# Kernel optimization log

Measured on AMD Instinct MI355X. Metric: run time of the kernel, lower is better.

The kernel has to match this reference:

```python
import jax, jax.numpy as jnp
import numpy as np

N = 100000  # nodes
NEG_SLOPE = 0.2


def gat_conv(x, W, att_src, att_dst, bias, src, dst):
    # x: [N, Fin], W: [Fin, Fout], att_*: [Fout], bias: [Fout]
    h = x @ W                                    # [N, Fout]
    a_s = h @ att_src                            # [N]
    a_d = h @ att_dst                            # [N]
    e = jax.nn.leaky_relu(a_s[src] + a_d[dst], NEG_SLOPE)  # [E]
    # segment softmax over destination-node neighborhoods
    m = jax.ops.segment_max(e, dst, num_segments=N)        # [N]
    ex = jnp.exp(e - m[dst])
    denom = jax.ops.segment_sum(ex, dst, num_segments=N)   # [N]
    alpha = ex / denom[dst]                      # [E]
    out = jax.ops.segment_sum(alpha[:, None] * h[src], dst, num_segments=N)
    return out + bias


def setup_inputs() -> dict:
    key = jax.random.key(0)
    ks = jax.random.split(key, 10)
    F_in, H, C, E = 512, 16, 40, 3200000
    x = jax.random.normal(ks[0], (N, F_in), dtype=jnp.float32)
    edge_index = jax.random.randint(ks[1], (2, E), 0, N, dtype=jnp.int64)
    s1 = 1.0 / np.sqrt(F_in)
    s2 = 1.0 / np.sqrt(H)
    return {
        "x": x,
        "W1": jax.random.normal(ks[2], (F_in, H), dtype=jnp.float32) * s1,
        "att_src1": jax.random.normal(ks[3], (H,), dtype=jnp.float32) * s2,
        "att_dst1": jax.random.normal(ks[4], (H,), dtype=jnp.float32) * s2,
        "bias1": jnp.zeros((H,), dtype=jnp.float32),
        "W2": jax.random.normal(ks[5], (H, C), dtype=jnp.float32) * s2,
        "att_src2": jax.random.normal(ks[6], (C,), dtype=jnp.float32) / np.sqrt(C),
        "att_dst2": jax.random.normal(ks[7], (C,), dtype=jnp.float32) / np.sqrt(C),
        "bias2": jnp.zeros((C,), dtype=jnp.float32),
        "edge_index": edge_index,
    }


def reference(x, W1, att_src1, att_dst1, bias1, W2, att_src2, att_dst2, bias2, edge_index):
    # add self loops (PyG GATConv default add_self_loops=True)
    loop = jnp.arange(N, dtype=edge_index.dtype)
    src = jnp.concatenate([edge_index[0], loop])
    dst = jnp.concatenate([edge_index[1], loop])
    h = gat_conv(x, W1, att_src1, att_dst1, bias1, src, dst)
    h = jax.nn.relu(h)  # dropout is identity in eval mode
    out = gat_conv(h, W2, att_src2, att_dst2, bias2, src, dst)
    return out
```

## Files before the change

kernel.cpp:

```cpp
#include <hip/hip_runtime.h>
#include <math.h>


constexpr int FIN = 512;
constexpr int F1  = 16;
constexpr int C2  = 40;
constexpr float SLOPE = 0.2f;
constexpr int BSH  = 8;
constexpr int NBMAX = 512;

__global__ __launch_bounds__(128) void k1_gemm(
    const float* __restrict__ x, const float* __restrict__ W1,
    const float* __restrict__ att_s, const float* __restrict__ att_d,
    float* __restrict__ h1, float* __restrict__ a_s, float* __restrict__ a_d, int n)
{
    __shared__ float WT[F1][FIN + 4];
    for (int idx = threadIdx.x; idx < FIN * F1; idx += 128) {
        int k = idx >> 4, o = idx & 15;
        WT[o][k] = W1[idx];
    }
    __syncthreads();

    const int o0 = (threadIdx.x & 3) * 4;
    const int ng = threadIdx.x >> 2;
    const int node0 = blockIdx.x * 128 + ng * 4;

    const float* xr[4];
#pragma unroll
    for (int nn = 0; nn < 4; ++nn) {
        int node = node0 + nn;
        xr[nn] = x + (size_t)(node < n ? node : 0) * FIN;
    }

    float acc[4][4] = {};
    for (int k = 0; k < FIN; k += 4) {
        float4 wv[4];
#pragma unroll
        for (int oo = 0; oo < 4; ++oo) wv[oo] = *(const float4*)&WT[o0 + oo][k];
#pragma unroll
        for (int nn = 0; nn < 4; ++nn) {
            float4 xv = *(const float4*)(xr[nn] + k);
#pragma unroll
            for (int oo = 0; oo < 4; ++oo)
                acc[nn][oo] += xv.x * wv[oo].x + xv.y * wv[oo].y +
                               xv.z * wv[oo].z + xv.w * wv[oo].w;
        }
    }

#pragma unroll
    for (int nn = 0; nn < 4; ++nn) {
        int node = node0 + nn;
        float ps = 0.f, pd = 0.f;
#pragma unroll
        for (int oo = 0; oo < 4; ++oo) {
            ps += acc[nn][oo] * att_s[o0 + oo];
            pd += acc[nn][oo] * att_d[o0 + oo];
        }
        ps += __shfl_xor(ps, 1); ps += __shfl_xor(ps, 2);
        pd += __shfl_xor(pd, 1); pd += __shfl_xor(pd, 2);
        if (node < n) {
            *(float4*)&h1[(size_t)node * F1 + o0] =
                make_float4(acc[nn][0], acc[nn][1], acc[nn][2], acc[nn][3]);
            if ((threadIdx.x & 3) == 0) { a_s[node] = ps; a_d[node] = pd; }
        }
    }
}

__global__ __launch_bounds__(256) void k_bhist(const int* __restrict__ dst,
                                               int* __restrict__ bcnt, int E, int nb)
{
    __shared__ int cnt[NBMAX];
    for (int t = threadIdx.x; t < NBMAX; t += 256) cnt[t] = 0;
    __syncthreads();
    int base = blockIdx.x * 4096;
#pragma unroll
    for (int k = 0; k < 16; ++k) {
        int e = base + k * 256 + threadIdx.x;
        if (e < E) atomicAdd(&cnt[dst[e] >> BSH], 1);
    }
    __syncthreads();
    for (int t = threadIdx.x; t < nb; t += 256) {
        int c = cnt[t];
        if (c) atomicAdd(&bcnt[t], c);
    }
}

__global__ __launch_bounds__(512) void k_bscan(const int* __restrict__ bcnt,
                                               int* __restrict__ bbase,
                                               int* __restrict__ gcur, int nb, int E)
{
    __shared__ int sc[512];
    int t = threadIdx.x;
    int v = (t < nb) ? bcnt[t] : 0;
    sc[t] = v; __syncthreads();
    for (int off = 1; off < 512; off <<= 1) {
        int u = (t >= off) ? sc[t - off] : 0;
        __syncthreads();
        sc[t] += u;
        __syncthreads();
    }
    int excl = sc[t] - v;
    if (t < nb) { bbase[t] = excl; gcur[t] = excl; }
    if (t == 0) bbase[nb] = E;
}

__global__ __launch_bounds__(256) void k_bucket(const int* __restrict__ src,
                                                const int* __restrict__ dst,
                                                int* __restrict__ gcur,
                                                unsigned int* __restrict__ bpk, int E)
{
    __shared__ int cnt[NBMAX];
    __shared__ int cur[NBMAX];
    for (int t = threadIdx.x; t < NBMAX; t += 256) cnt[t] = 0;
    __syncthreads();
    int base = blockIdx.x * 4096;
#pragma unroll
    for (int k = 0; k < 16; ++k) {
        int e = base + k * 256 + threadIdx.x;
        if (e < E) atomicAdd(&cnt[dst[e] >> BSH], 1);
    }
    __syncthreads();
    for (int t = threadIdx.x; t < NBMAX; t += 256) {
        int c = cnt[t];
        cur[t] = c ? atomicAdd(&gcur[t], c) : 0;
    }
    __syncthreads();
#pragma unroll
    for (int k = 0; k < 16; ++k) {
        int e = base + k * 256 + threadIdx.x;
        if (e < E) {
            int d = dst[e];
            int b = d >> BSH;
            int pos = atomicAdd(&cur[b], 1);
            bpk[pos] = (unsigned)src[e] | ((unsigned)(d & ((1 << BSH) - 1)) << 17);
        }
    }
}

__global__ __launch_bounds__(256) void k_refine(const unsigned int* __restrict__ bpk,
                                                const int* __restrict__ bbase,
                                                int* __restrict__ offs,
                                                int* __restrict__ ssrc, int n, int E)
{
    __shared__ int cnt[256];
    __shared__ int sc[256];
    int b = blockIdx.x;
    int beg = bbase[b], end = bbase[b + 1];
    int t = threadIdx.x;
    cnt[t] = 0;
    __syncthreads();
    for (int j = beg + t; j < end; j += 256)
        atomicAdd(&cnt[(bpk[j] >> 17) & 255], 1);
    __syncthreads();
    int v = cnt[t];
    sc[t] = v; __syncthreads();
    for (int off = 1; off < 256; off <<= 1) {
        int u = (t >= off) ? sc[t - off] : 0;
        __syncthreads();
        sc[t] += u;
        __syncthreads();
    }
    int excl = sc[t] - v;
    int node = (b << BSH) + t;
    if (node < n) offs[node] = beg + excl;
    __syncthreads();
    cnt[t] = excl;
    __syncthreads();
    for (int j = beg + t; j < end; j += 256) {
        unsigned pk = bpk[j];
        int local = (pk >> 17) & 255;
        int pos = atomicAdd(&cnt[local], 1);
        ssrc[beg + pos] = (int)(pk & 0x1FFFFu);
    }
    if (b == (int)gridDim.x - 1 && t == 0) offs[n] = E;
}

__global__ __launch_bounds__(256) void g1_gather(
    const int* __restrict__ offs, const int* __restrict__ ssrc,
    const float* __restrict__ h1, const float* __restrict__ a_s, const float* __restrict__ a_d,
    const float* __restrict__ bias1, const float* __restrict__ W2,
    const float* __restrict__ att_s2, const float* __restrict__ att_d2,
    float* __restrict__ hin2, float* __restrict__ pa_s, float* __restrict__ pa_d, int n)
{
    __shared__ float vs[F1], vd[F1];
    if (threadIdx.x < 32) {
        int f = threadIdx.x & 15;
        const float* att = (threadIdx.x < 16) ? att_s2 : att_d2;
        float sum = 0.f;
        for (int c = 0; c < C2; ++c) sum += W2[f * C2 + c] * att[c];
        if (threadIdx.x < 16) vs[f] = sum; else vd[f] = sum;
    }
    __syncthreads();
    const int g = threadIdx.x >> 4, f = threadIdx.x & 15;
    const int i = blockIdx.x * 16 + g;
    if (i >= n) return;
    const float adi = a_d[i];
    float acc = 0.f, dacc = 0.f;
    const int jb = offs[i], je = offs[i + 1];
    for (int j0 = jb; j0 < je; j0 += 16) {
        const int rem = je - j0;
        int se = ssrc[(f < rem) ? j0 + f : jb];
        float ev = a_s[se] + adi;
        ev = (ev >= 0.f) ? ev : SLOPE * ev;
        float pex = (f < rem) ? __expf(ev) : 0.f;
        dacc += pex;
        if (rem >= 16) {
#pragma unroll
            for (int t = 0; t < 16; ++t) {
                int s = __shfl(se, t, 16);
                float ex = __shfl(pex, t, 16);
                acc += ex * h1[(size_t)s * F1 + f];
            }
        } else {
            for (int t = 0; t < rem; ++t) {
                int s = __shfl(se, t, 16);
                float ex = __shfl(pex, t, 16);
                acc += ex * h1[(size_t)s * F1 + f];
            }
        }
    }
    float evs = a_s[i] + adi;
    evs = (evs >= 0.f) ? evs : SLOPE * evs;
    float exs = __expf(evs);
    acc += exs * h1[(size_t)i * F1 + f];
    float den = dacc;
#pragma unroll
    for (int o = 1; o < 16; o <<= 1) den += __shfl_xor(den, o);
    den += exs;
    float val = fmaxf(acc / den + bias1[f], 0.f);
    hin2[(size_t)i * F1 + f] = val;
    float ps = val * vs[f], pd = val * vd[f];
#pragma unroll
    for (int o = 1; o < 16; o <<= 1) { ps += __shfl_xor(ps, o); pd += __shfl_xor(pd, o); }
    if (f == 0) { pa_s[i] = ps; pa_d[i] = pd; }
}

__global__ __launch_bounds__(256) void g2_gather(
    const int* __restrict__ offs, const int* __restrict__ ssrc,
    const float* __restrict__ hin2, const float* __restrict__ a_s, const float* __restrict__ a_d,
    const float* __restrict__ W2, const float* __restrict__ bias2,
    float* __restrict__ out, int n)
{
    __shared__ float W2s[F1 * 41];
    __shared__ float vals[16][17];
    for (int idx = threadIdx.x; idx < F1 * C2; idx += 256)
        W2s[(idx / C2) * 41 + (idx % C2)] = W2[idx];
    __syncthreads();
    const int g = threadIdx.x >> 4, f = threadIdx.x & 15;
    const int i = blockIdx.x * 16 + g;
    if (i >= n) return;
    const float adi = a_d[i];
    float acc = 0.f, dacc = 0.f;
    const int jb = offs[i], je = offs[i + 1];
    for (int j0 = jb; j0 < je; j0 += 16) {
        const int rem = je - j0;
        int se = ssrc[(f < rem) ? j0 + f : jb];
        float ev = a_s[se] + adi;
        ev = (ev >= 0.f) ? ev : SLOPE * ev;
        float pex = (f < rem) ? __expf(ev) : 0.f;
        dacc += pex;
        if (rem >= 16) {
#pragma unroll
            for (int t = 0; t < 16; ++t) {
                int s = __shfl(se, t, 16);
                float ex = __shfl(pex, t, 16);
                acc += ex * hin2[(size_t)s * F1 + f];
            }
        } else {
            for (int t = 0; t < rem; ++t) {
                int s = __shfl(se, t, 16);
                float ex = __shfl(pex, t, 16);
                acc += ex * hin2[(size_t)s * F1 + f];
            }
        }
    }
    float evs = a_s[i] + adi;
    evs = (evs >= 0.f) ? evs : SLOPE * evs;
    float exs = __expf(evs);
    acc += exs * hin2[(size_t)i * F1 + f];
    float den = dacc;
#pragma unroll
    for (int o = 1; o < 16; o <<= 1) den += __shfl_xor(den, o);
    den += exs;
    vals[g][f] = acc / den;
    for (int c = f; c < C2; c += 16) {
        float r = bias2[c];
#pragma unroll
        for (int ff = 0; ff < F1; ++ff) r += vals[g][ff] * W2s[ff * 41 + c];
        out[(size_t)i * C2 + c] = r;
    }
}

extern "C" void kernel_launch(void* const* d_in, const int* in_sizes, int n_in,
                              void* d_out, int out_size, void* d_ws, size_t ws_size,
                              hipStream_t stream) {
    const float* x      = (const float*)d_in[0];
    const float* W1     = (const float*)d_in[1];
    const float* att_s1 = (const float*)d_in[2];
    const float* att_d1 = (const float*)d_in[3];
    const float* bias1  = (const float*)d_in[4];
    const float* W2     = (const float*)d_in[5];
    const float* att_s2 = (const float*)d_in[6];
    const float* att_d2 = (const float*)d_in[7];
    const float* bias2  = (const float*)d_in[8];
    const int*   edge   = (const int*)d_in[9];

    const int n = in_sizes[0] / FIN;
    const int E = in_sizes[9] / 2;
    const int* src = edge;
    const int* dst = edge + E;
    const int NBK = (n + (1 << BSH) - 1) >> BSH;

    size_t Ns = (size_t)n, Es = (size_t)E;
    int*   ssrc  = (int*)d_ws;
    int*   offs  = ssrc + Es;
    int*   bcnt  = offs + Ns + 1;
    int*   bbase = bcnt + NBMAX;
    int*   gcur  = bbase + NBMAX + 1;
    unsigned int* bpk = (unsigned int*)(gcur + NBMAX);
    float* h1    = (float*)bpk;
    float* a_s1  = h1   + 16 * Ns;
    float* a_d1  = a_s1 + Ns;
    float* hin2  = a_d1 + Ns;
    float* pa_s2 = hin2 + 16 * Ns;
    float* pa_d2 = pa_s2 + Ns;
    float* out   = (float*)d_out;

    const int gbA = (E + 4095) / 4096;
    const int gb1 = (n + 127) / 128;
    const int gbg = (n + 15) / 16;

    hipMemsetAsync(bcnt, 0, sizeof(int) * NBMAX, stream);
    k_bhist <<<gbA, 256, 0, stream>>>(dst, bcnt, E, NBK);
    k_bscan <<<1, 512, 0, stream>>>(bcnt, bbase, gcur, NBK, E);
    k_bucket<<<gbA, 256, 0, stream>>>(src, dst, gcur, bpk, E);
    k_refine<<<NBK, 256, 0, stream>>>(bpk, bbase, offs, ssrc, n, E);
    k1_gemm <<<gb1, 128, 0, stream>>>(x, W1, att_s1, att_d1, h1, a_s1, a_d1, n);
    g1_gather<<<gbg, 256, 0, stream>>>(offs, ssrc, h1, a_s1, a_d1, bias1, W2,
                                       att_s2, att_d2, hin2, pa_s2, pa_d2, n);
    g2_gather<<<gbg, 256, 0, stream>>>(offs, ssrc, hin2, pa_s2, pa_d2, W2, bias2, out, n);
}
```

Baseline: 613.8 us.

## Fuse per-bucket CSR refine into aggregation kernels using LDS-local edge lists

Removes the separate refine kernel that wrote a global CSR. Each aggregation kernel now rebuilds its bucket's per-node edge list in shared memory, with one thread per node accumulating all 16 features using float4 loads. It falls back to scanning the whole bucket when the edge count exceeds LDS capacity. This drops the global ssrc/offs writes and reads, but the bucket sort is redone twice. With only NBK (~391) blocks of 256 threads and about 40KB of LDS each, occupancy and load balance may suffer, and the per-thread serial loops follow skewed degrees.

```diff
diff --git a/kernel.cpp b/kernel.cpp
--- a/kernel.cpp
+++ b/kernel.cpp
@@ -6,8 +6,9 @@
 constexpr int F1  = 16;
 constexpr int C2  = 40;
 constexpr float SLOPE = 0.2f;
-constexpr int BSH  = 8;
+constexpr int BSH   = 8;
 constexpr int NBMAX = 512;
+constexpr int LDSE  = 9728;
 
 __global__ __launch_bounds__(128) void k1_gemm(
     const float* __restrict__ x, const float* __restrict__ W1,
@@ -137,157 +138,245 @@
     }
 }
 
-__global__ __launch_bounds__(256) void k_refine(const unsigned int* __restrict__ bpk,
-                                                const int* __restrict__ bbase,
-                                                int* __restrict__ offs,
-                                                int* __restrict__ ssrc, int n, int E)
-{
-    __shared__ int cnt[256];
-    __shared__ int sc[256];
-    int b = blockIdx.x;
-    int beg = bbase[b], end = bbase[b + 1];
-    int t = threadIdx.x;
-    cnt[t] = 0;
-    __syncthreads();
-    for (int j = beg + t; j < end; j += 256)
-        atomicAdd(&cnt[(bpk[j] >> 17) & 255], 1);
-    __syncthreads();
-    int v = cnt[t];
-    sc[t] = v; __syncthreads();
-    for (int off = 1; off < 256; off <<= 1) {
-        int u = (t >= off) ? sc[t - off] : 0;
-        __syncthreads();
-        sc[t] += u;
-        __syncthreads();
-    }
-    int excl = sc[t] - v;
-    int node = (b << BSH) + t;
-    if (node < n) offs[node] = beg + excl;
-    __syncthreads();
-    cnt[t] = excl;
-    __syncthreads();
-    for (int j = beg + t; j < end; j += 256) {
-        unsigned pk = bpk[j];
-        int local = (pk >> 17) & 255;
-        int pos = atomicAdd(&cnt[local], 1);
-        ssrc[beg + pos] = (int)(pk & 0x1FFFFu);
-    }
-    if (b == (int)gridDim.x - 1 && t == 0) offs[n] = E;
-}
-
-__global__ __launch_bounds__(256) void g1_gather(
-    const int* __restrict__ offs, const int* __restrict__ ssrc,
+__global__ __launch_bounds__(256) void f1_agg(
+    const unsigned int* __restrict__ bpk, const int* __restrict__ bbase,
     const float* __restrict__ h1, const float* __restrict__ a_s, const float* __restrict__ a_d,
     const float* __restrict__ bias1, const float* __restrict__ W2,
     const float* __restrict__ att_s2, const float* __restrict__ att_d2,
     float* __restrict__ hin2, float* __restrict__ pa_s, float* __restrict__ pa_d, int n)
 {
-    __shared__ float vs[F1], vd[F1];
-    if (threadIdx.x < 32) {
-        int f = threadIdx.x & 15;
-        const float* att = (threadIdx.x < 16) ? att_s2 : att_d2;
+    __shared__ int lsrc[LDSE];
+    __shared__ int cnt[256];
+    __shared__ int scn[256];
+    __shared__ float vs[F1], vd[F1], bl[F1];
+    const int b = blockIdx.x, t = threadIdx.x;
+    const int beg = bbase[b], end = bbase[b + 1];
+    const int m = end - beg;
+
+    if (t < 32) {
+        int f = t & 15;
+        const float* att = (t < 16) ? att_s2 : att_d2;
         float sum = 0.f;
         for (int c = 0; c < C2; ++c) sum += W2[f * C2 + c] * att[c];
-        if (threadIdx.x < 16) vs[f] = sum; else vd[f] = sum;
-    }
-    __syncthreads();
-    const int g = threadIdx.x >> 4, f = threadIdx.x & 15;
-    const int i = blockIdx.x * 16 + g;
-    if (i >= n) return;
-    const float adi = a_d[i];
-    float acc = 0.f, dacc = 0.f;
-    const int jb = offs[i], je = offs[i + 1];
-    for (int j0 = jb; j0 < je; j0 += 16) {
-        const int rem = je - j0;
-        int se = ssrc[(f < rem) ? j0 + f : jb];
-        float ev = a_s[se] + adi;
-        ev = (ev >= 0.f) ? ev : SLOPE * ev;
-        float pex = (f < rem) ? __expf(ev) : 0.f;
-        dacc += pex;
-        if (rem >= 16) {
-#pragma unroll
-            for (int t = 0; t < 16; ++t) {
-                int s = __shfl(se, t, 16);
-                float ex = __shfl(pex, t, 16);
-                acc += ex * h1[(size_t)s * F1 + f];
+        if (t < 16) vs[f] = sum; else vd[f] = sum;
+    } else if (t < 48) {
+        bl[t - 32] = bias1[t - 32];
+    }
+    cnt[t] = 0;
+    __syncthreads();
+
+    int myBeg = 0, myCnt = 0;
+    const bool fits = (m <= LDSE);
+    if (fits) {
+        for (int j = beg + t; j < end; j += 256)
+            atomicAdd(&cnt[(bpk[j] >> 17) & 255], 1);
+        __syncthreads();
+        int v = cnt[t];
+        scn[t] = v;
+        __syncthreads();
+        for (int off = 1; off < 256; off <<= 1) {
+            int u = (t >= off) ? scn[t - off] : 0;
+            __syncthreads();
+            scn[t] += u;
+            __syncthreads();
+        }
+        myCnt = v;
+        myBeg = scn[t] - v;
+        cnt[t] = myBeg;
+        __syncthreads();
+        for (int j = beg + t; j < end; j += 256) {
+            unsigned pk = bpk[j];
+            int p = atomicAdd(&cnt[(pk >> 17) & 255], 1);
+            lsrc[p] = (int)(pk & 0x1FFFFu);
+        }
+        __syncthreads();
+    }
+
+    const int node = (b << BSH) + t;
+    if (node >= n) return;
+
+    const float adi = a_d[node];
+    float acc[F1];
+#pragma unroll
+    for (int f = 0; f < F1; ++f) acc[f] = 0.f;
+    float den = 0.f;
+
+    if (fits) {
+        for (int k = 0; k < myCnt; ++k) {
+            int s = lsrc[myBeg + k];
+            float ev = a_s[s] + adi;
+            ev = (ev >= 0.f) ? ev : SLOPE * ev;
+            float ex = __expf(ev);
+            den += ex;
+            const float4* hp = (const float4*)(h1 + (size_t)s * F1);
+#pragma unroll
+            for (int q = 0; q < 4; ++q) {
+                float4 v = hp[q];
+                acc[4*q+0] += ex * v.x; acc[4*q+1] += ex * v.y;
+                acc[4*q+2] += ex * v.z; acc[4*q+3] += ex * v.w;
             }
-        } else {
-            for (int t = 0; t < rem; ++t) {
-                int s = __shfl(se, t, 16);
-                float ex = __shfl(pex, t, 16);
-                acc += ex * h1[(size_t)s * F1 + f];
+        }
+    } else {
+        for (int j = beg; j < end; ++j) {
+            unsigned pk = bpk[j];
+            if ((int)((pk >> 17) & 255) != t) continue;
+            int s = (int)(pk & 0x1FFFFu);
+            float ev = a_s[s] + adi;
+            ev = (ev >= 0.f) ? ev : SLOPE * ev;
+            float ex = __expf(ev);
+            den += ex;
+            const float4* hp = (const float4*)(h1 + (size_t)s * F1);
+#pragma unroll
+            for (int q = 0; q < 4; ++q) {
+                float4 v = hp[q];
+                acc[4*q+0] += ex * v.x; acc[4*q+1] += ex * v.y;
+                acc[4*q+2] += ex * v.z; acc[4*q+3] += ex * v.w;
             }
         }
     }
-    float evs = a_s[i] + adi;
+
+    float evs = a_s[node] + adi;
     evs = (evs >= 0.f) ? evs : SLOPE * evs;
     float exs = __expf(evs);
-    acc += exs * h1[(size_t)i * F1 + f];
-    float den = dacc;
-#pragma unroll
-    for (int o = 1; o < 16; o <<= 1) den += __shfl_xor(den, o);
-    den += exs;
-    float val = fmaxf(acc / den + bias1[f], 0.f);
-    hin2[(size_t)i * F1 + f] = val;
-    float ps = val * vs[f], pd = val * vd[f];
-#pragma unroll
-    for (int o = 1; o < 16; o <<= 1) { ps += __shfl_xor(ps, o); pd += __shfl_xor(pd, o); }
-    if (f == 0) { pa_s[i] = ps; pa_d[i] = pd; }
-}
-
-__global__ __launch_bounds__(256) void g2_gather(
-    const int* __restrict__ offs, const int* __restrict__ ssrc,
+    const float4* hs = (const float4*)(h1 + (size_t)node * F1);
+    float inv;
+    {
+        float d2 = den + exs;
+        inv = 1.f / d2;
+    }
+    float ps = 0.f, pd = 0.f;
+    float4* ho = (float4*)(hin2 + (size_t)node * F1);
+#pragma unroll
+    for (int q = 0; q < 4; ++q) {
+        float4 sv = hs[q];
+        float4 V;
+        V.x = fmaxf((acc[4*q+0] + exs * sv.x) * inv + bl[4*q+0], 0.f);
+        V.y = fmaxf((acc[4*q+1] + exs * sv.y) * inv + bl[4*q+1], 0.f);
+        V.z = fmaxf((acc[4*q+2] + exs * sv.z) * inv + bl[4*q+2], 0.f);
+        V.w = fmaxf((acc[4*q+3] + exs * sv.w) * inv + bl[4*q+3], 0.f);
+        ho[q] = V;
+        ps += V.x * vs[4*q+0] + V.y * vs[4*q+1] + V.z * vs[4*q+2] + V.w * vs[4*q+3];
+        pd += V.x * vd[4*q+0] + V.y * vd[4*q+1] + V.z * vd[4*q+2] + V.w * vd[4*q+3];
+    }
+    pa_s[node] = ps; pa_d[node] = pd;
+}
+
+__global__ __launch_bounds__(256) void f2_agg(
+    const unsigned int* __restrict__ bpk, const int* __restrict__ bbase,
     const float* __restrict__ hin2, const float* __restrict__ a_s, const float* __restrict__ a_d,
     const float* __restrict__ W2, const float* __restrict__ bias2,
     float* __restrict__ out, int n)
 {
-    __shared__ float W2s[F1 * 41];
-    __shared__ float vals[16][17];
-    for (int idx = threadIdx.x; idx < F1 * C2; idx += 256)
-        W2s[(idx / C2) * 41 + (idx % C2)] = W2[idx];
-    __syncthreads();
-    const int g = threadIdx.x >> 4, f = threadIdx.x & 15;
-    const int i = blockIdx.x * 16 + g;
-    if (i >= n) return;
-    const float adi = a_d[i];
-    float acc = 0.f, dacc = 0.f;
-    const int jb = offs[i], je = offs[i + 1];
-    for (int j0 = jb; j0 < je; j0 += 16) {
-        const int rem = je - j0;
-        int se = ssrc[(f < rem) ? j0 + f : jb];
-        float ev = a_s[se] + adi;
-        ev = (ev >= 0.f) ? ev : SLOPE * ev;
-        float pex = (f < rem) ? __expf(ev) : 0.f;
-        dacc += pex;
-        if (rem >= 16) {
-#pragma unroll
-            for (int t = 0; t < 16; ++t) {
-                int s = __shfl(se, t, 16);
-                float ex = __shfl(pex, t, 16);
-                acc += ex * hin2[(size_t)s * F1 + f];
+    __shared__ int lsrc[LDSE];
+    __shared__ int cnt[256];
+    __shared__ int scn[256];
+    __shared__ float W2s[F1 * C2];
+    __shared__ float b2[C2];
+    const int b = blockIdx.x, t = threadIdx.x;
+    const int beg = bbase[b], end = bbase[b + 1];
+    const int m = end - beg;
+
+    for (int idx = t; idx < F1 * C2; idx += 256) W2s[idx] = W2[idx];
+    if (t < C2) b2[t] = bias2[t];
+    cnt[t] = 0;
+    __syncthreads();
+
+    int myBeg = 0, myCnt = 0;
+    const bool fits = (m <= LDSE);
+    if (fits) {
+        for (int j = beg + t; j < end; j += 256)
+            atomicAdd(&cnt[(bpk[j] >> 17) & 255], 1);
+        __syncthreads();
+        int v = cnt[t];
+        scn[t] = v;
+        __syncthreads();
+        for (int off = 1; off < 256; off <<= 1) {
+            int u = (t >= off) ? scn[t - off] : 0;
+            __syncthreads();
+            scn[t] += u;
+            __syncthreads();
+        }
+        myCnt = v;
+        myBeg = scn[t] - v;
+        cnt[t] = myBeg;
+        __syncthreads();
+        for (int j = beg + t; j < end; j += 256) {
+            unsigned pk = bpk[j];
+            int p = atomicAdd(&cnt[(pk >> 17) & 255], 1);
+            lsrc[p] = (int)(pk & 0x1FFFFu);
+        }
+        __syncthreads();
+    }
+
+    const int node = (b << BSH) + t;
+    if (node >= n) return;
+
+    const float adi = a_d[node];
+    float acc[F1];
+#pragma unroll
+    for (int f = 0; f < F1; ++f) acc[f] = 0.f;
+    float den = 0.f;
+
+    if (fits) {
+        for (int k = 0; k < myCnt; ++k) {
+            int s = lsrc[myBeg + k];
+            float ev = a_s[s] + adi;
+            ev = (ev >= 0.f) ? ev : SLOPE * ev;
+            float ex = __expf(ev);
+            den += ex;
+            const float4* hp = (const float4*)(hin2 + (size_t)s * F1);
+#pragma unroll
+            for (int q = 0; q < 4; ++q) {
+                float4 v = hp[q];
+                acc[4*q+0] += ex * v.x; acc[4*q+1] += ex * v.y;
+                acc[4*q+2] += ex * v.z; acc[4*q+3] += ex * v.w;
             }
-        } else {
-            for (int t = 0; t < rem; ++t) {
-                int s = __shfl(se, t, 16);
-                float ex = __shfl(pex, t, 16);
-                acc += ex * hin2[(size_t)s * F1 + f];
+        }
+    } else {
+        for (int j = beg; j < end; ++j) {
+            unsigned pk = bpk[j];
+            if ((int)((pk >> 17) & 255) != t) continue;
+            int s = (int)(pk & 0x1FFFFu);
+            float ev = a_s[s] + adi;
+            ev = (ev >= 0.f) ? ev : SLOPE * ev;
+            float ex = __expf(ev);
+            den += ex;
+            const float4* hp = (const float4*)(hin2 + (size_t)s * F1);
+#pragma unroll
+            for (int q = 0; q < 4; ++q) {
+                float4 v = hp[q];
+                acc[4*q+0] += ex * v.x; acc[4*q+1] += ex * v.y;
+                acc[4*q+2] += ex * v.z; acc[4*q+3] += ex * v.w;
             }
         }
     }
-    float evs = a_s[i] + adi;
+
+    float evs = a_s[node] + adi;
     evs = (evs >= 0.f) ? evs : SLOPE * evs;
     float exs = __expf(evs);
-    acc += exs * hin2[(size_t)i * F1 + f];
-    float den = dacc;
-#pragma unroll
-    for (int o = 1; o < 16; o <<= 1) den += __shfl_xor(den, o);
-    den += exs;
-    vals[g][f] = acc / den;
-    for (int c = f; c < C2; c += 16) {
-        float r = bias2[c];
-#pragma unroll
-        for (int ff = 0; ff < F1; ++ff) r += vals[g][ff] * W2s[ff * 41 + c];
-        out[(size_t)i * C2 + c] = r;
+    const float4* hs = (const float4*)(hin2 + (size_t)node * F1);
+    float inv = 1.f / (den + exs);
+    float val[F1];
+#pragma unroll
+    for (int q = 0; q < 4; ++q) {
+        float4 sv = hs[q];
+        val[4*q+0] = (acc[4*q+0] + exs * sv.x) * inv;
+        val[4*q+1] = (acc[4*q+1] + exs * sv.y) * inv;
+        val[4*q+2] = (acc[4*q+2] + exs * sv.z) * inv;
+        val[4*q+3] = (acc[4*q+3] + exs * sv.w) * inv;
+    }
+    float* op = out + (size_t)node * C2;
+    for (int c0 = 0; c0 < C2; c0 += 4) {
+        float4 r = make_float4(b2[c0], b2[c0+1], b2[c0+2], b2[c0+3]);
+#pragma unroll
+        for (int f = 0; f < F1; ++f) {
+            float v = val[f];
+            r.x += v * W2s[f * C2 + c0 + 0];
+            r.y += v * W2s[f * C2 + c0 + 1];
+            r.z += v * W2s[f * C2 + c0 + 2];
+            r.w += v * W2s[f * C2 + c0 + 3];
+        }
+        *(float4*)(op + c0) = r;
     }
 }
 
@@ -311,32 +400,28 @@
     const int* dst = edge + E;
     const int NBK = (n + (1 << BSH) - 1) >> BSH;
 
-    size_t Ns = (size_t)n, Es = (size_t)E;
-    int*   ssrc  = (int*)d_ws;
-    int*   offs  = ssrc + Es;
-    int*   bcnt  = offs + Ns + 1;
+    size_t Ns = (size_t)n;
+    float* h1    = (float*)d_ws;
+    float* hin2  = h1   + 16 * Ns;
+    float* a_s1  = hin2 + 16 * Ns;
+    float* a_d1  = a_s1 + Ns;
+    float* pa_s2 = a_d1 + Ns;
+    float* pa_d2 = pa_s2 + Ns;
+    int*   bcnt  = (int*)(pa_d2 + Ns);
     int*   bbase = bcnt + NBMAX;
     int*   gcur  = bbase + NBMAX + 1;
     unsigned int* bpk = (unsigned int*)(gcur + NBMAX);
-    float* h1    = (float*)bpk;
-    float* a_s1  = h1   + 16 * Ns;
-    float* a_d1  = a_s1 + Ns;
-    float* hin2  = a_d1 + Ns;
-    float* pa_s2 = hin2 + 16 * Ns;
-    float* pa_d2 = pa_s2 + Ns;
     float* out   = (float*)d_out;
 
     const int gbA = (E + 4095) / 4096;
     const int gb1 = (n + 127) / 128;
-    const int gbg = (n + 15) / 16;
 
     hipMemsetAsync(bcnt, 0, sizeof(int) * NBMAX, stream);
     k_bhist <<<gbA, 256, 0, stream>>>(dst, bcnt, E, NBK);
     k_bscan <<<1, 512, 0, stream>>>(bcnt, bbase, gcur, NBK, E);
     k_bucket<<<gbA, 256, 0, stream>>>(src, dst, gcur, bpk, E);
-    k_refine<<<NBK, 256, 0, stream>>>(bpk, bbase, offs, ssrc, n, E);
     k1_gemm <<<gb1, 128, 0, stream>>>(x, W1, att_s1, att_d1, h1, a_s1, a_d1, n);
-    g1_gather<<<gbg, 256, 0, stream>>>(offs, ssrc, h1, a_s1, a_d1, bias1, W2,
-                                       att_s2, att_d2, hin2, pa_s2, pa_d2, n);
-    g2_gather<<<gbg, 256, 0, stream>>>(offs, ssrc, hin2, pa_s2, pa_d2, W2, bias2, out, n);
-}
+    f1_agg  <<<NBK, 256, 0, stream>>>(bpk, bbase, h1, a_s1, a_d1, bias1, W2,
+                                      att_s2, att_d2, hin2, pa_s2, pa_d2, n);
+    f2_agg  <<<NBK, 256, 0, stream>>>(bpk, bbase, hin2, pa_s2, pa_d2, W2, bias2, out, n);
+}
```

Result: faster. 587.4 us (-4.3%).
